# Kernel optimization log

Measured on AMD Instinct MI355X. Metric: run time of the kernel, lower is better.

Reference implementation:

```python
import math
import jax, jax.numpy as jnp
import numpy as np


def setup_inputs() -> dict:
    key = jax.random.key(0)
    ks = jax.random.split(key, 5)
    B, T, C = 4, 2048, 1024
    H = 16
    s = 0.02
    return {
        "x": jax.random.normal(ks[0], (B, T, C), dtype=jnp.float32),
        "W_attn": jax.random.normal(ks[1], (C, 3 * C), dtype=jnp.float32) * s,
        "b_attn": jax.random.normal(ks[2], (3 * C,), dtype=jnp.float32) * s,
        "W_proj": jax.random.normal(ks[3], (C, C), dtype=jnp.float32) * s,
        "b_proj": jax.random.normal(ks[4], (C,), dtype=jnp.float32) * s,
        "n_head": 16,
    }


def reference(x, W_attn, b_attn, W_proj, b_proj, n_head):
    B, T, C = x.shape
    hd = C // n_head
    qkv = x @ W_attn + b_attn  # (B,T,3C)
    q, k, v = jnp.split(qkv, 3, axis=-1)
    # (B,H,T,hd)
    q = q.reshape(B, T, n_head, hd).transpose(0, 2, 1, 3)
    k = k.reshape(B, T, n_head, hd).transpose(0, 2, 1, 3)
    v = v.reshape(B, T, n_head, hd).transpose(0, 2, 1, 3)
    # ||q-k||^2 = |q|^2 + |k|^2 - 2 q.k  (GEMM form, avoids (B,H,T,T,hd) diff tensor)
    q2 = jnp.sum(q * q, axis=-1)[..., :, None]  # (B,H,T,1)
    k2 = jnp.sum(k * k, axis=-1)[..., None, :]  # (B,H,1,T)
    qk = jnp.einsum("bhqd,bhkd->bhqk", q, k)    # (B,H,T,T)
    sq_l2 = q2 + k2 - 2.0 * qk
    scale = -1.0 / (2.0 * math.sqrt(hd))
    scores = jnp.exp(sq_l2 * scale)
    causal = jnp.tril(jnp.ones((T, T), dtype=bool))  # (T,T)
    scores = jnp.where(causal[None, None, :, :], scores, 0.0)
    y = jnp.einsum("bhqk,bhkd->bhqd", scores, v)  # (B,H,T,hd)
    y = y.transpose(0, 2, 1, 3).reshape(B, T, C)
    return y @ W_proj + b_proj
```

## Files before the change

### kernel.cpp

```cpp
#include <hip/hip_runtime.h>

typedef __bf16 bf16;
typedef __bf16 bf16x8 __attribute__((ext_vector_type(8)));
typedef __bf16 bf16x4 __attribute__((ext_vector_type(4)));
typedef float floatx4 __attribute__((ext_vector_type(4)));

#define MFMA_BF16(a, b, c) __builtin_amdgcn_mfma_f32_16x16x32_bf16((a), (b), (c), 0, 0, 0)

#define GLOAD_LDS16(gp, lp)                                      \
  __builtin_amdgcn_global_load_lds(                              \
      (const __attribute__((address_space(1))) void*)(gp),       \
      (__attribute__((address_space(3))) void*)(lp), 16, 0, 0)

#define SEQ_T 2048
#define DIM_C 1024
#define HDIM 64
#define MROWS 8192
#define N_QKV 3072

__global__ __launch_bounds__(256) void f32_to_bf16(
    const float* __restrict__ in, bf16* __restrict__ out) {
  const size_t i = ((size_t)blockIdx.x * 256 + threadIdx.x) * 8;
  const float4 f0 = *(const float4*)&in[i];
  const float4 f1 = *(const float4*)&in[i + 4];
  bf16x8 v;
  v[0] = (bf16)f0.x; v[1] = (bf16)f0.y; v[2] = (bf16)f0.z; v[3] = (bf16)f0.w;
  v[4] = (bf16)f1.x; v[5] = (bf16)f1.y; v[6] = (bf16)f1.z; v[7] = (bf16)f1.w;
  *(bf16x8*)&out[i] = v;
}

__global__ __launch_bounds__(256) void transpose_f32_bf16(
    const float* __restrict__ in, bf16* __restrict__ out, int R, int C) {
  __shared__ bf16 tile[32][33];
  const int bx = blockIdx.x * 32, by = blockIdx.y * 32;
  const int tx = threadIdx.x & 31, ty = threadIdx.x >> 5;
  for (int i = 0; i < 32; i += 8)
    tile[ty + i][tx] = (bf16)in[(size_t)(by + ty + i) * C + bx + tx];
  __syncthreads();
  for (int i = 0; i < 32; i += 8)
    out[(size_t)(bx + ty + i) * R + by + tx] = tile[tx][ty + i];
}

__global__ __launch_bounds__(256) void scale_transpose_v(
    const bf16* __restrict__ qkv, bf16* __restrict__ VT) {
  const int bh = blockIdx.x;
  const int kt = blockIdx.y;
  const int bb = bh >> 4, h = bh & 15;
  const int tid = threadIdx.x;
  __shared__ bf16 tile[64][72];
  const int r0 = tid >> 3, c8 = (tid & 7) << 3;
  const float c2 = -0.09016844f;
  for (int i = 0; i < 2; i++) {
    const int r = r0 + i * 32;
    const size_t gr = (size_t)bb * SEQ_T + kt * 64 + r;
    const bf16x8 kv = *(const bf16x8*)&qkv[gr * N_QKV + 1024 + h * HDIM + c8];
    float s = 0.f;
    for (int j = 0; j < 8; j++) { const float f = (float)kv[j]; s += f * f; }
    s += __shfl_xor(s, 1); s += __shfl_xor(s, 2); s += __shfl_xor(s, 4);
    const float vscale = exp2f(s * c2);
    const bf16x8 vv = *(const bf16x8*)&qkv[gr * N_QKV + 2048 + h * HDIM + c8];
    for (int j = 0; j < 8; j++)
      tile[c8 + j][r ^ c8] = (bf16)((float)vv[j] * vscale);
  }
  __syncthreads();
  for (int i = 0; i < 2; i++) {
    const int u = i * 256 + tid;
    const int d = u >> 3, kc = (u & 7) << 3;
    const bf16x8 ov = *(const bf16x8*)&tile[d][kc ^ (d & 0x38)];
    *(bf16x8*)&VT[(size_t)bh * 131072 + (size_t)d * 2048 + kt * 64 + kc] = ov;
  }
}

template <typename OT>
__global__ __launch_bounds__(256) void gemm_lds(
    const bf16* __restrict__ A,
    const bf16* __restrict__ Bt,
    const float* __restrict__ bias,
    OT* __restrict__ Cout,
    int M, int N, int K, int lda) {
  __shared__ __align__(16) bf16 Asl[128 * 64];
  __shared__ __align__(16) bf16 Bsl[128 * 64];
  const int bm = blockIdx.y * 128, bn = blockIdx.x * 128;
  const int tid = threadIdx.x;
  const int wave = tid >> 6, lane = tid & 63;
  const int wm = (wave >> 1) * 64, wn = (wave & 1) * 64;
  const int quad = lane >> 4, l16 = lane & 15;

  const floatx4 zero = {0.f, 0.f, 0.f, 0.f};
  floatx4 acc[4][4];
  for (int i = 0; i < 4; i++)
    for (int j = 0; j < 4; j++) acc[i][j] = zero;

  const bf16 *gA[4], *gB[4];
  bf16 *lA[4], *lB[4];
  for (int i = 0; i < 4; i++) {
    const int s = i * 256 + tid;
    const int row = s >> 3;
    const int c = (s & 7) ^ (row & 7);
    gA[i] = &A[(size_t)(bm + row) * lda + c * 8];
    gB[i] = &Bt[(size_t)(bn + row) * K + c * 8];
    lA[i] = &Asl[(i * 256 + wave * 64) * 8];
    lB[i] = &Bsl[(i * 256 + wave * 64) * 8];
  }

  for (int k0 = 0; k0 < K; k0 += 64) {
    for (int i = 0; i < 4; i++) GLOAD_LDS16(gA[i] + k0, lA[i]);
    for (int i = 0; i < 4; i++) GLOAD_LDS16(gB[i] + k0, lB[i]);
    __syncthreads();
    for (int kk = 0; kk < 2; kk++) {
      bf16x8 af[4], bfr[4];
      for (int it = 0; it < 4; it++) {
        const int row = wm + it * 16 + l16;
        const int phys = (kk * 4 + quad) ^ (row & 7);
        af[it] = *(const bf16x8*)&Asl[row * 64 + phys * 8];
      }
      for (int jt = 0; jt < 4; jt++) {
        const int row = wn + jt * 16 + l16;
        const int phys = (kk * 4 + quad) ^ (row & 7);
        bfr[jt] = *(const bf16x8*)&Bsl[row * 64 + phys * 8];
      }
      for (int it = 0; it < 4; it++)
        for (int jt = 0; jt < 4; jt++)
          acc[it][jt] = MFMA_BF16(af[it], bfr[jt], acc[it][jt]);
    }
    __syncthreads();
  }
  for (int jt = 0; jt < 4; jt++) {
    const int col = bn + wn + jt * 16 + l16;
    const float bv = bias[col];
    for (int it = 0; it < 4; it++)
      for (int r = 0; r < 4; r++) {
        const int row = bm + wm + it * 16 + quad * 4 + r;
        Cout[(size_t)row * N + col] = (OT)(acc[it][jt][r] + bv);
      }
  }
}

__global__ __launch_bounds__(256, 4) void attn_kernel(
    bf16* __restrict__ qkv,
    const bf16* __restrict__ VT) {
  const int p = blockIdx.y;
  const int bh = blockIdx.x;
  const int bb = bh >> 4, h = bh & 15;
  const int qtA = p, qtB = 31 - p;
  const int tid = threadIdx.x;
  const int wave = tid >> 6, lane = tid & 63;
  const int quad = lane >> 4, l16 = lane & 15;

  __shared__ __align__(16) bf16 Ps[128][72];
  __shared__ __align__(16) bf16 Ksl[2][64 * 64];
  __shared__ __align__(16) bf16 Vsl[2][64 * 64];
  __shared__ float q2c[128];

  const size_t rowbase = (size_t)bb * SEQ_T;
  const float c2 = -0.09016844f;
  const float m2c2 = 0.18033688f;

  bf16x8 aq[2][2];
  for (int T = 0; T < 2; T++) {
    const int qt = T ? qtB : qtA;
    const size_t grow = rowbase + qt * 64 + wave * 16 + l16;
    float s = 0.f;
    for (int ks = 0; ks < 2; ks++) {
      aq[T][ks] = *(const bf16x8*)&qkv[grow * N_QKV + h * HDIM + ks * 32 + quad * 8];
      for (int j = 0; j < 8; j++) { const float f = (float)aq[T][ks][j]; s += f * f; }
    }
    s += __shfl_xor(s, 16); s += __shfl_xor(s, 32);
    if (quad == 0) q2c[T * 64 + wave * 16 + l16] = s * c2;
  }

  const floatx4 zero = {0.f, 0.f, 0.f, 0.f};
  floatx4 accy[2][4];
  for (int T = 0; T < 2; T++)
    for (int jt = 0; jt < 4; jt++) accy[T][jt] = zero;

  const int r0 = tid >> 3;
  const int cb = (tid & 7) ^ (r0 & 7);
  const bf16* gK = &qkv[(rowbase + r0) * N_QKV + 1024 + h * HDIM + cb * 8];
  const bf16* gV = &VT[(size_t)bh * 131072 + (size_t)r0 * 2048 + cb * 8];

#define STAGE(kt_, nb_) do {                                            \
    const size_t ko = (size_t)(kt_) * 64 * N_QKV;                       \
    const int vo = (kt_) * 64;                                          \
    GLOAD_LDS16(gK + ko,                    &Ksl[nb_][(wave * 64) * 8]);\
    GLOAD_LDS16(gK + ko + (size_t)32 * N_QKV,                           \
                &Ksl[nb_][(256 + wave * 64) * 8]);                      \
    GLOAD_LDS16(gV + vo,                    &Vsl[nb_][(wave * 64) * 8]);\
    GLOAD_LDS16(gV + vo + 32 * 2048,        &Vsl[nb_][(256 + wave * 64) * 8]);\
  } while (0)

  STAGE(0, 0);
  int cur = 0;
  const int qrow = wave * 16 + l16;

  for (int kt = 0; kt <= qtB; kt++) {
    const bool actA = (kt <= qtA);
    __syncthreads();
    if (kt < qtB) STAGE(kt + 1, cur ^ 1);
    const bf16* Kb = Ksl[cur];
    const bf16* Vb = Vsl[cur];

    bf16x8 bk[4][2];
    for (int jt = 0; jt < 4; jt++)
      for (int ks = 0; ks < 2; ks++) {
        const int phys = (ks * 4 + quad) ^ (l16 & 7);
        bk[jt][ks] = *(const bf16x8*)&Kb[(jt * 16 + l16) * 64 + phys * 8];
      }
    floatx4 accs[2][4];
    for (int T = 0; T < 2; T++)
      for (int jt = 0; jt < 4; jt++) accs[T][jt] = zero;
    for (int T = 0; T < 2; T++) {
      if (T == 0 && !actA) continue;
      for (int ks = 0; ks < 2; ks++)
        for (int jt = 0; jt < 4; jt++)
          accs[T][jt] = MFMA_BF16(bk[jt][ks], aq[T][ks], accs[T][jt]);
    }

    for (int T = 0; T < 2; T++) {
      if (T == 0 && !actA) continue;
      const bool diag = (kt == (T == 0 ? qtA : qtB));
      for (int jt = 0; jt < 4; jt++) {
        const int kb = jt * 16 + quad * 4;
        bf16x4 pw;
        for (int r = 0; r < 4; r++) {
          float pe = exp2f(m2c2 * accs[T][jt][r]);
          if (diag && kb + r > qrow) pe = 0.f;
          pw[r] = (bf16)pe;
        }
        *(bf16x4*)&Ps[T * 64 + qrow][kb] = pw;
      }
    }

    bf16x8 bv[4][2];
    for (int dt = 0; dt < 4; dt++)
      for (int ks = 0; ks < 2; ks++) {
        const int phys = (ks * 4 + quad) ^ (l16 & 7);
        bv[dt][ks] = *(const bf16x8*)&Vb[(dt * 16 + l16) * 64 + phys * 8];
      }
    for (int T = 0; T < 2; T++) {
      if (T == 0 && !actA) continue;
      for (int ks = 0; ks < 2; ks++) {
        const bf16x8 ap =
            *(const bf16x8*)&Ps[T * 64 + qrow][ks * 32 + quad * 8];
        for (int jt = 0; jt < 4; jt++)
          accy[T][jt] = MFMA_BF16(ap, bv[jt][ks], accy[T][jt]);
      }
    }
    cur ^= 1;
  }
#undef STAGE

  for (int T = 0; T < 2; T++) {
    const int qt = (T == 0) ? qtA : qtB;
    float ysc[4];
    for (int r = 0; r < 4; r++)
      ysc[r] = exp2f(q2c[T * 64 + wave * 16 + quad * 4 + r]);
    for (int jt = 0; jt < 4; jt++) {
      const int col = h * HDIM + jt * 16 + l16;
      for (int r = 0; r < 4; r++) {
        const int ml = wave * 16 + quad * 4 + r;
        qkv[(rowbase + qt * 64 + ml) * N_QKV + 2048 + col] =
            (bf16)(accy[T][jt][r] * ysc[r]);
      }
    }
  }
}

extern "C" void kernel_launch(void* const* d_in, const int* in_sizes, int n_in,
                              void* d_out, int out_size, void* d_ws, size_t ws_size,
                              hipStream_t stream) {
  const float* x      = (const float*)d_in[0];
  const float* W_attn = (const float*)d_in[1];
  const float* b_attn = (const float*)d_in[2];
  const float* W_proj = (const float*)d_in[3];
  const float* b_proj = (const float*)d_in[4];
  float* out = (float*)d_out;

  char* ws = (char*)d_ws;
  bf16* qkv = (bf16*)(ws);
  bf16* VTb = (bf16*)(ws + 50331648);
  bf16* WaT = (bf16*)(ws + 67108864);
  bf16* WpT = (bf16*)(ws + 73400320);
  bf16* xb  = VTb;

  f32_to_bf16<<<dim3(4096), 256, 0, stream>>>(x, xb);
  transpose_f32_bf16<<<dim3(96, 32), 256, 0, stream>>>(W_attn, WaT, 1024, 3072);
  transpose_f32_bf16<<<dim3(32, 32), 256, 0, stream>>>(W_proj, WpT, 1024, 1024);
  gemm_lds<bf16><<<dim3(24, 64), 256, 0, stream>>>(
      xb, WaT, b_attn, qkv, MROWS, N_QKV, DIM_C, DIM_C);
  scale_transpose_v<<<dim3(64, 32), 256, 0, stream>>>(qkv, VTb);
  attn_kernel<<<dim3(64, 16), 256, 0, stream>>>(qkv, VTb);
  gemm_lds<float><<<dim3(8, 64), 256, 0, stream>>>(
      qkv + 2048, WpT, b_proj, out, MROWS, DIM_C, DIM_C, N_QKV);
}
```

Before: 289.5 us.

## Shrink and swizzle P buffer, fuse per-tile QK/PV loops, drop q2 LDS

The P scratch in shared memory is shrunk from two padded 64x72 tiles to one XOR-swizzled 64x64 tile, which is reused for each query tile in turn. The QK^T, exp, and PV steps now run back to back per query tile, and V fragments are loaded together with K. The q-norm scale is kept in registers and broadcast with shuffles instead of going through shared memory. This cuts LDS footprint, which may allow more blocks per CU, and avoids padding and bank conflicts, but it serializes reuse of the single P buffer across tiles within the wave.

```diff
diff --git a/kernel.cpp b/kernel.cpp
--- a/kernel.cpp
+++ b/kernel.cpp
@@ -147,16 +147,16 @@
   const int wave = tid >> 6, lane = tid & 63;
   const int quad = lane >> 4, l16 = lane & 15;
 
-  __shared__ __align__(16) bf16 Ps[128][72];
+  __shared__ __align__(16) bf16 Ps[64 * 64];
   __shared__ __align__(16) bf16 Ksl[2][64 * 64];
   __shared__ __align__(16) bf16 Vsl[2][64 * 64];
-  __shared__ float q2c[128];
 
   const size_t rowbase = (size_t)bb * SEQ_T;
   const float c2 = -0.09016844f;
   const float m2c2 = 0.18033688f;
 
   bf16x8 aq[2][2];
+  float sq[2];
   for (int T = 0; T < 2; T++) {
     const int qt = T ? qtB : qtA;
     const size_t grow = rowbase + qt * 64 + wave * 16 + l16;
@@ -166,7 +166,7 @@
       for (int j = 0; j < 8; j++) { const float f = (float)aq[T][ks][j]; s += f * f; }
     }
     s += __shfl_xor(s, 16); s += __shfl_xor(s, 32);
-    if (quad == 0) q2c[T * 64 + wave * 16 + l16] = s * c2;
+    sq[T] = s;
   }
 
   const floatx4 zero = {0.f, 0.f, 0.f, 0.f};
@@ -192,6 +192,7 @@
   STAGE(0, 0);
   int cur = 0;
   const int qrow = wave * 16 + l16;
+  const int rk = l16 & 7;
 
   for (int kt = 0; kt <= qtB; kt++) {
     const bool actA = (kt <= qtA);
@@ -200,48 +201,38 @@
     const bf16* Kb = Ksl[cur];
     const bf16* Vb = Vsl[cur];
 
-    bf16x8 bk[4][2];
+    bf16x8 bk[4][2], bv[4][2];
     for (int jt = 0; jt < 4; jt++)
       for (int ks = 0; ks < 2; ks++) {
-        const int phys = (ks * 4 + quad) ^ (l16 & 7);
+        const int phys = (ks * 4 + quad) ^ rk;
         bk[jt][ks] = *(const bf16x8*)&Kb[(jt * 16 + l16) * 64 + phys * 8];
-      }
-    floatx4 accs[2][4];
-    for (int T = 0; T < 2; T++)
-      for (int jt = 0; jt < 4; jt++) accs[T][jt] = zero;
+        bv[jt][ks] = *(const bf16x8*)&Vb[(jt * 16 + l16) * 64 + phys * 8];
+      }
+
     for (int T = 0; T < 2; T++) {
       if (T == 0 && !actA) continue;
+      floatx4 accs[4];
+      for (int jt = 0; jt < 4; jt++) accs[jt] = zero;
       for (int ks = 0; ks < 2; ks++)
         for (int jt = 0; jt < 4; jt++)
-          accs[T][jt] = MFMA_BF16(bk[jt][ks], aq[T][ks], accs[T][jt]);
-    }
-
-    for (int T = 0; T < 2; T++) {
-      if (T == 0 && !actA) continue;
+          accs[jt] = MFMA_BF16(bk[jt][ks], aq[T][ks], accs[jt]);
+
       const bool diag = (kt == (T == 0 ? qtA : qtB));
       for (int jt = 0; jt < 4; jt++) {
         const int kb = jt * 16 + quad * 4;
         bf16x4 pw;
         for (int r = 0; r < 4; r++) {
-          float pe = exp2f(m2c2 * accs[T][jt][r]);
+          float pe = exp2f(m2c2 * accs[jt][r]);
           if (diag && kb + r > qrow) pe = 0.f;
           pw[r] = (bf16)pe;
         }
-        *(bf16x4*)&Ps[T * 64 + qrow][kb] = pw;
-      }
-    }
-
-    bf16x8 bv[4][2];
-    for (int dt = 0; dt < 4; dt++)
+        const int ch = (2 * jt + (quad >> 1)) ^ rk;
+        *(bf16x4*)&Ps[qrow * 64 + ch * 8 + (quad & 1) * 4] = pw;
+      }
+
       for (int ks = 0; ks < 2; ks++) {
-        const int phys = (ks * 4 + quad) ^ (l16 & 7);
-        bv[dt][ks] = *(const bf16x8*)&Vb[(dt * 16 + l16) * 64 + phys * 8];
-      }
-    for (int T = 0; T < 2; T++) {
-      if (T == 0 && !actA) continue;
-      for (int ks = 0; ks < 2; ks++) {
-        const bf16x8 ap =
-            *(const bf16x8*)&Ps[T * 64 + qrow][ks * 32 + quad * 8];
+        const int ch = (ks * 4 + quad) ^ rk;
+        const bf16x8 ap = *(const bf16x8*)&Ps[qrow * 64 + ch * 8];
         for (int jt = 0; jt < 4; jt++)
           accy[T][jt] = MFMA_BF16(ap, bv[jt][ks], accy[T][jt]);
       }
@@ -254,7 +245,7 @@
     const int qt = (T == 0) ? qtA : qtB;
     float ysc[4];
     for (int r = 0; r < 4; r++)
-      ysc[r] = exp2f(q2c[T * 64 + wave * 16 + quad * 4 + r]);
+      ysc[r] = exp2f(__shfl(sq[T], quad * 4 + r) * c2);
     for (int jt = 0; jt < 4; jt++) {
       const int col = h * HDIM + jt * 16 + l16;
       for (int r = 0; r < 4; r++) {
```

Result: slower. 302.0 us (+4.3%).
